# Performance work log

Hardware: AMD Instinct MI355X
Metric: run time of the kernel (lower is better)

The kernel has to match this reference:

```python
import jax, jax.numpy as jnp
import numpy as np

EMBED = 128; HEADS = 4; NUM_CLASSES = 20; NUM_LAYERS = 2
SCENE = (128, 128, 16)
NQ = SCENE[0] * SCENE[1] * SCENE[2]
NI = 300
IMG = (96, 320); ORI = (384, 1280)
VOXEL_SIZE = 0.2
SCORE_THR, MASK_THR, IOU_THR = 0.25, 0.5, 0.8


def _image_grid():
    # generate_grid(image_shape, ori_image_shape), then flip(dims=[0]) -> (x, y) pixel coords in ori resolution
    ys = jnp.arange(IMG[0], dtype=jnp.float32) * (ORI[0] / IMG[0])
    xs = jnp.arange(IMG[1], dtype=jnp.float32) * (ORI[1] / IMG[1])
    gy, gx = jnp.meshgrid(ys, xs, indexing='ij')
    return jnp.stack([gx, gy], 0)  # (2, h, w)


def _scene_pos():
    g = jnp.stack(jnp.meshgrid(*[jnp.arange(s, dtype=jnp.float32) for s in SCENE], indexing='ij'), 0)
    g = (g + 0.5) * VOXEL_SIZE  # project_scale = 1
    return g.reshape(3, -1).T  # (NQ, 3)


def _layernorm(x, g, b):
    mu = x.mean(-1, keepdims=True)
    var = ((x - mu) ** 2).mean(-1, keepdims=True)
    return (x - mu) * jax.lax.rsqrt(var + 1e-5) * g + b


def _mha(q, k, v, w, b):
    # w: (4, D, D) = Wq, Wk, Wv, Wo; b: (4, D)
    B, Nq, D = q.shape; hd = D // HEADS
    def proj(x, i):
        return (x @ w[i].T + b[i]).reshape(B, -1, HEADS, hd).transpose(0, 2, 1, 3)
    qh, kh, vh = proj(q, 0), proj(k, 1), proj(v, 2)
    attn = jax.nn.softmax(jnp.einsum('bhqd,bhkd->bhqk', qh, kh) / jnp.sqrt(jnp.float32(hd)), axis=-1)
    o = jnp.einsum('bhqk,bhkd->bhqd', attn, vh).transpose(0, 2, 1, 3).reshape(B, Nq, D)
    return o @ w[3].T + b[3]


def _tlayer(q, k, v, aw, ab, lg, lb, w1, b1, w2, b2):
    x = _layernorm(q + _mha(q, k, v, aw, ab), lg[0], lb[0])
    h = jax.nn.relu(x @ w1.T + b1) @ w2.T + b2
    return _layernorm(x + h, lg[1], lb[1])


def setup_inputs():
    key = jax.random.key(0)
    ks = jax.random.split(key, 20)
    h, w = IMG
    queries = jax.random.normal(ks[0], (1, NI, EMBED), jnp.float32)
    # 8 instances get a strong class logit so exactly they pass score_thr
    pred_logits = 0.1 * jax.random.normal(ks[1], (1, NI, NUM_CLASSES + 1), jnp.float32)
    ii = jnp.arange(8)
    pred_logits = pred_logits.at[0, ii, ii % (NUM_CLASSES + 1)].add(6.0)
    # each kept instance owns a disjoint 40-px-wide strip -> passes IoU>=0.8
    pred_masks = -6.0 + 0.1 * jax.random.normal(ks[2], (1, NI, h, w), jnp.float32)
    strip = jnp.arange(w) // 40  # 0..7
    boost = 12.0 * (jnp.arange(NI)[:, None] == strip[None, :]).astype(jnp.float32)
    pred_masks = pred_masks + boost[None, :, None, :]
    x3d = 0.1 * jax.random.normal(ks[3], (1, EMBED) + SCENE, jnp.float32)
    depth = 1.0 + 49.0 * jax.random.uniform(ks[4], (1, h, w), jnp.float32)
    K = jnp.array([[[500.0, 0.0, 160.0], [0.0, 500.0, 48.0], [0.0, 0.0, 1.0]]], jnp.float32)
    E = jnp.array([[[1.0, 0.0, 0.0, 0.5], [0.0, 1.0, 0.0, 1.0], [0.0, 0.0, 1.0, 1.5], [0.0, 0.0, 0.0, 1.0]]], jnp.float32)
    voxel_origin = jnp.array([[[0.0, -12.8, -2.0]]], jnp.float32)
    fov_mask = jax.random.bernoulli(ks[5], 0.25, (1, NQ))
    L = NUM_LAYERS
    scene_embed_w = 0.02 * jax.random.normal(ks[6], (NQ, EMBED), jnp.float32)
    inst_pos_w = 0.02 * jax.random.normal(ks[7], (NI, EMBED), jnp.float32)
    pos_w = 0.02 * jax.random.normal(ks[8], (EMBED, 3), jnp.float32)
    conv_w = 0.05 * jax.random.normal(ks[9], (NUM_CLASSES, EMBED), jnp.float32)
    conv_b = jnp.zeros((NUM_CLASSES,), jnp.float32)
    attn_w = 0.05 * jax.random.normal(ks[10], (L, 2, 4, EMBED, EMBED), jnp.float32)
    attn_b = jnp.zeros((L, 2, 4, EMBED), jnp.float32)
    ln_g = jnp.ones((L, 2, 2, EMBED), jnp.float32)
    ln_b = jnp.zeros((L, 2, 2, EMBED), jnp.float32)
    ffn_w1 = 0.05 * jax.random.normal(ks[11], (L, 2, 4 * EMBED, EMBED), jnp.float32)
    ffn_b1 = jnp.zeros((L, 2, 4 * EMBED), jnp.float32)
    ffn_w2 = 0.05 * jax.random.normal(ks[12], (L, 2, EMBED, 4 * EMBED), jnp.float32)
    ffn_b2 = jnp.zeros((L, 2, EMBED), jnp.float32)
    return dict(queries=queries, pred_logits=pred_logits, pred_masks=pred_masks, x3d=x3d, depth=depth,
                K=K, E=E, voxel_origin=voxel_origin, fov_mask=fov_mask,
                scene_embed_w=scene_embed_w, inst_pos_w=inst_pos_w, pos_w=pos_w, conv_w=conv_w, conv_b=conv_b,
                attn_w=attn_w, attn_b=attn_b, ln_g=ln_g, ln_b=ln_b,
                ffn_w1=ffn_w1, ffn_b1=ffn_b1, ffn_w2=ffn_w2, ffn_b2=ffn_b2)


def reference(queries, pred_logits, pred_masks, x3d, depth, K, E, voxel_origin, fov_mask,
              scene_embed_w, inst_pos_w, pos_w, conv_w, conv_b,
              attn_w, attn_b, ln_g, ln_b, ffn_w1, ffn_b1, ffn_w2, ffn_b2):
    h, w = IMG
    # ---- panoptic_postprocess (bs == 1) ----
    sig = jax.nn.sigmoid(pred_logits[0])
    prob_cls = jax.nn.softmax(sig / 0.06, axis=-1)
    scores = prob_cls.max(-1); labels = prob_cls.argmax(-1)
    keep = (labels != prob_cls.shape[-1]) & (scores > SCORE_THR)
    kidx = jnp.nonzero(keep)[0]
    pm = jax.nn.sigmoid(pred_masks[0])[kidx]          # (k, h, w)
    sk = scores[kidx]
    mids = (sk[:, None, None] * pm).argmax(0)          # per-pixel winning instance
    masks = mids[None] == jnp.arange(pm.shape[0])[:, None, None]
    marea = masks.reshape(pm.shape[0], -1).sum(1)
    pmb = pm >= MASK_THR
    parea = pmb.reshape(pm.shape[0], -1).sum(1)
    masks = masks & pmb
    keep_ = (masks.reshape(pm.shape[0], -1).sum(1) > 0) & (marea / parea >= IOU_THR)
    sel = jnp.nonzero(keep_)[0]
    inst_masks = masks[sel]                             # (k2, h, w)
    k2idx = kidx[sel]                                   # final kept slots in [0, NI)
    # ---- gather_mask_pos (depth already at (h, w) -> interpolate is identity) ----
    ig = _image_grid()
    ig3 = jnp.concatenate([ig[None] * depth[:, None], depth[:, None]], axis=1)  # (1,3,h,w) = (x*d, y*d, d)
    cam = jnp.linalg.inv(K) @ ig3.reshape(1, 3, -1)
    homo = jnp.concatenate([cam, jnp.ones((1, 1, h * w), cam.dtype)], axis=1)
    world = (jnp.linalg.inv(E) @ homo)[0, :3].T        # (hw, 3)
    xyz = inst_masks.reshape(inst_masks.shape[0], -1).astype(world.dtype) @ world  # masked sum per instance
    mask_pos = xyz @ pos_w.T                            # Linear(3, embed, bias=False)
    inst_q = queries[0][k2idx][None]                    # (1, k2, D)
    inst_p = (inst_pos_w[k2idx] + mask_pos)[None]
    # ---- scene tokens ----
    scene_embed_full = scene_embed_w[None] + x3d.reshape(1, EMBED, NQ).transpose(0, 2, 1)
    qsrc = scene_embed_full
    fidx = jnp.nonzero(fov_mask[0])[0]
    se = scene_embed_full[:, fidx]
    sp = ((_scene_pos()[None] + voxel_origin)[:, fidx]) @ pos_w.T
    for i in range(NUM_LAYERS):
        inst_q = _tlayer(inst_q + inst_p, se + sp, se, attn_w[i, 0], attn_b[i, 0], ln_g[i, 0], ln_b[i, 0],
                         ffn_w1[i, 0], ffn_b1[i, 0], ffn_w2[i, 0], ffn_b2[i, 0])
        se = _tlayer(se + sp, inst_q + inst_p, inst_q, attn_w[i, 1], attn_b[i, 1], ln_g[i, 1], ln_b[i, 1],
                     ffn_w1[i, 1], ffn_b1[i, 1], ffn_w2[i, 1], ffn_b2[i, 1])
    # ---- index_fov_back_to_voxels + cls_head (project_scale==1 -> Identity + 1x1 Conv3d) ----
    full = qsrc.at[:, fidx].set(se)
    x3d_ = full.transpose(0, 2, 1).reshape(1, EMBED, *SCENE)
    out = jnp.einsum('bcxyz,oc->boxyz', x3d_, conv_w) + conv_b.reshape(1, -1, 1, 1, 1)
    return out
```

## Files before the change

### kernel.cpp

```cpp
#include <hip/hip_runtime.h>
#include <math.h>

#define EMBED 128
#define NCLS 21
#define NI_ 300
#define IMH 96
#define IMW 320
#define NPIX (IMH*IMW)
#define NQ 262144
#define NF_MAX 73728
#define INST_MAX 16
#define IH_MAX 64
#define RS32 0.17677669529663687f

#define S_NF 0
#define S_NK 1
#define S_NINST 2
#define S_NIH 3
#define S_INVK 8
#define S_INVE 24
#define S_KIDX 64
#define S_SKK 400
#define S_MAREA 768
#define S_PAREA 1088
#define S_AREA2 1408
#define S_XYZ 1728
#define S_SELJ 2656
#define S_K2 2688
#define S_FCNT 3072
#define S_FOFF 3328
#define S_INSTQ 4096
#define S_INSTP 6144
#define S_QIN 8192
#define S_QH 10240
#define S_XI 12288
#define S_KHB 16384
#define S_VHB 18432
#define S_QKT 20480
#define S_SB 28672
#define S_SUMV 28928
#define S_WSUM 29056

#define OFF_FIDX ((size_t)1<<20)
#define OFF_INV  ((size_t)2<<20)
#define OFF_W1T  ((size_t)3<<20)
#define OFF_W2T  (((size_t)3<<20) + 512*128*4)
#define OFF_SE   ((size_t)4<<20)
#define SE_BYTES ((size_t)NF_MAX*128*4)
#define OFF_A1   (OFF_SE + SE_BYTES)
#define OFF_A2   (OFF_A1 + SE_BYTES)
#define OFF_SC   (OFF_A2 + SE_BYTES)

__global__ __launch_bounds__(256) void k_init(const float* Km, const float* Em, float* ws){
  int* iw = (int*)ws;
  for (int i = threadIdx.x; i < 4096; i += 256) iw[i] = 0;
  __syncthreads();
  if (threadIdx.x == 0){
    float* fw = ws;
    const float* K = Km;
    float A = K[4]*K[8]-K[5]*K[7];
    float B = K[5]*K[6]-K[3]*K[8];
    float C = K[3]*K[7]-K[4]*K[6];
    float det = K[0]*A + K[1]*B + K[2]*C;
    float id = 1.0f/det;
    fw[S_INVK+0] = A*id;
    fw[S_INVK+1] = (K[2]*K[7]-K[1]*K[8])*id;
    fw[S_INVK+2] = (K[1]*K[5]-K[2]*K[4])*id;
    fw[S_INVK+3] = B*id;
    fw[S_INVK+4] = (K[0]*K[8]-K[2]*K[6])*id;
    fw[S_INVK+5] = (K[2]*K[3]-K[0]*K[5])*id;
    fw[S_INVK+6] = C*id;
    fw[S_INVK+7] = (K[1]*K[6]-K[0]*K[7])*id;
    fw[S_INVK+8] = (K[0]*K[4]-K[1]*K[3])*id;
    float M[4][8];
    for (int r=0;r<4;r++){ for(int c=0;c<4;c++){ M[r][c]=Em[r*4+c]; M[r][4+c]=(r==c)?1.f:0.f; } }
    for (int col=0; col<4; col++){
      int piv=col; float best=fabsf(M[col][col]);
      for (int r=col+1;r<4;r++){ float v=fabsf(M[r][col]); if(v>best){best=v;piv=r;} }
      if (piv!=col){ for(int c=0;c<8;c++){ float tmp=M[col][c]; M[col][c]=M[piv][c]; M[piv][c]=tmp; } }
      float inv=1.0f/M[col][col];
      for (int c=0;c<8;c++) M[col][c]*=inv;
      for (int r=0;r<4;r++){ if(r==col) continue; float f=M[r][col]; for(int c=0;c<8;c++) M[r][c]-=f*M[col][c]; }
    }
    for (int r=0;r<4;r++) for(int c=0;c<4;c++) fw[S_INVE+r*4+c]=M[r][4+c];
  }
}

__global__ __launch_bounds__(320) void k_score(const float* logits, float* ws){
  int* iw=(int*)ws; float* fw=ws;
  __shared__ float ssc[NI_];
  __shared__ int skp[NI_];
  int t=threadIdx.x;
  if (t < NI_){
    float v[NCLS]; float mx=-1e30f;
    for (int c=0;c<NCLS;c++){
      float l=logits[t*NCLS+c];
      float sg=1.0f/(1.0f+expf(-l));
      float x=sg/0.06f;
      v[c]=x; mx=fmaxf(mx,x);
    }
    float s=0.f;
    for (int c=0;c<NCLS;c++) s += expf(v[c]-mx);
    float score=1.0f/s;
    ssc[t]=score; skp[t]=(score>0.25f)?1:0;
  }
  __syncthreads();
  if (t==0){
    int nk=0;
    for (int i=0;i<NI_;i++){ if(skp[i]){ iw[S_KIDX+nk]=i; fw[S_SKK+nk]=ssc[i]; nk++; } }
    iw[S_NK]=nk;
  }
}

__global__ __launch_bounds__(256) void k_winner(const float* pmask, const float* depth, float* ws){
  int* iw=(int*)ws; float* fw=ws;
  int nk=iw[S_NK];
  if (nk>NI_) nk=NI_;
  __shared__ int s_pa[NI_], s_ma[NI_], s_a2[NI_];
  __shared__ float s_x[NI_], s_y[NI_], s_z[NI_];
  __shared__ int s_gi[NI_];
  __shared__ float s_sc[NI_];
  int t=threadIdx.x;
  int lane=t&63;
  for (int j=t;j<nk;j+=256){
    s_pa[j]=0; s_ma[j]=0; s_a2[j]=0;
    s_x[j]=0.f; s_y[j]=0.f; s_z[j]=0.f;
    s_gi[j]=iw[S_KIDX+j]; s_sc[j]=fw[S_SKK+j];
  }
  __syncthreads();
// ... 60 lines not shown
    fw[S_INSTP+idx]=instposw[gi*128+e]+mp;
  }
}

__global__ __launch_bounds__(256) void k_fov_count(const int* fov, float* ws){
  int* iw=(int*)ws;
  __shared__ int red[256];
  int t=threadIdx.x;
  int base=blockIdx.x*1024;
  int s=0;
  for (int k=0;k<4;k++) s += (fov[base+k*256+t]!=0)?1:0;
  red[t]=s; __syncthreads();
  for (int st=128;st>0;st>>=1){ if(t<st) red[t]+=red[t+st]; __syncthreads(); }
  if (t==0) iw[S_FCNT+blockIdx.x]=red[0];
}

__global__ void k_fov_scan(float* ws){
  int* iw=(int*)ws;
  if (threadIdx.x==0){
    int acc=0;
    for (int b=0;b<256;b++){ iw[S_FOFF+b]=acc; acc+=iw[S_FCNT+b]; }
    iw[S_NF]=(acc<NF_MAX)?acc:NF_MAX;
  }
}

__global__ __launch_bounds__(256) void k_fov_scatter(const int* fov, float* ws){
  int* iw=(int*)ws;
  int* fidx=(int*)((char*)ws+OFF_FIDX);
  int* invr=(int*)((char*)ws+OFF_INV);
  __shared__ int wsums[4];
  __shared__ int woff[4];
  __shared__ int cur;
  __shared__ int tot;
  int t=threadIdx.x; int w=t>>6; int lane=t&63;
  if (t==0) cur=iw[S_FOFF+blockIdx.x];
  __syncthreads();
  int base=blockIdx.x*1024;
  for (int k=0;k<4;k++){
    int i=base+k*256+t;
    int f=(fov[i]!=0)?1:0;
    unsigned long long m=__ballot(f);
    int rk=__popcll(m & ((lane==0)?0ull:((~0ull)>>(64-lane))));
    if (lane==0) wsums[w]=__popcll(m);
    __syncthreads();
    if (t==0){ int a=0; for(int q2=0;q2<4;q2++){ woff[q2]=a; a+=wsums[q2]; } tot=a; }
    __syncthreads();
    if (f){
      int r=cur+woff[w]+rk;
      if (r<NF_MAX){ fidx[r]=i; invr[i]=r; } else invr[i]=-1;
    } else invr[i]=-1;
    __syncthreads();
    if (t==0) cur+=tot;
    __syncthreads();
  }
}

__global__ __launch_bounds__(256) void k_se_build(const float* sew, const float* x3d, const int* fidx, float* SE, float* ws){
  int* iw=(int*)ws;
  int nf=iw[S_NF];
  int r0=blockIdx.x*64;
  if (r0>=nf) return;
  int nr=min(64,nf-r0);
  __shared__ float tile[64][129];
  __shared__ int fidxl[64];
  int t=threadIdx.x;
  if (t<64) fidxl[t]=(t<nr)? fidx[r0+t]:0;
  __syncthreads();
  for (int idx=t; idx<64*128; idx+=256){
    int v=idx>>7, e=idx&127;
    tile[v][e]=(v<nr)? sew[(size_t)fidxl[v]*128+e]:0.f;
  }
  __syncthreads();
  for (int idx=t; idx<128*64; idx+=256){
    int c=idx>>6, v=idx&63;
    if (v<nr) tile[v][c]+=x3d[(size_t)c*NQ+fidxl[v]];
  }
  __syncthreads();
  for (int idx=t; idx<64*128; idx+=256){
    int v=idx>>7, e=idx&127;
    if (v<nr) SE[(r0+v)*128+e]=tile[v][e];
  }
}

__global__ __launch_bounds__(256) void kA_prep(const float* Wq, const float* bq, const float* Wk, const float* bk, float* ws){
  int* iw=(int*)ws; float* fw=ws;
  int n=iw[S_NINST]; int nih=iw[S_NIH];
  int t=threadIdx.x;
  for (int idx=t; idx<n*128; idx+=256) fw[S_QIN+idx]=fw[S_INSTQ+idx]+fw[S_INSTP+idx];
  __syncthreads();
  for (int idx=t; idx<n*128; idx+=256){
    int i=idx>>7, e=idx&127;
    float a=bq[e];
    for (int k=0;k<128;k++) a+=fw[S_QIN+i*128+k]*Wq[e*128+k];
    fw[S_QH+idx]=a;
  }
  __syncthreads();
  for (int idx=t; idx<nih*128; idx+=256){
    int ih=idx>>7, e=idx&127;
    int i=ih>>2, h=ih&3;
    float a=0.f;
    for (int d=0;d<32;d++) a+=fw[S_QH+i*128+h*32+d]*Wk[(h*32+d)*128+e];
    fw[S_QKT+idx]=a*RS32;
  }
  for (int ih=t; ih<nih; ih+=256){
    int i=ih>>2, h=ih&3;
    float a=0.f;
    for (int d=0;d<32;d++) a+=fw[S_QH+i*128+h*32+d]*bk[h*32+d];
    fw[S_SB+ih]=a*RS32;
  }
}

__global__ __launch_bounds__(256) void kS1(const float* SE, float* SC, const float* posw, const float* org, const int* fidx, float* ws){
  int* iw=(int*)ws; float* fw=ws;
  int nf=iw[S_NF]; int nih=iw[S_NIH];
  int r0=blockIdx.x*64;
  if (r0>=nf || nih==0) return;
  int nr=min(64,nf-r0);
  __shared__ float xt[64][132];
  __shared__ float qk[64][132];
  __shared__ float sbl[64];
  __shared__ float pwl[384];
  __shared__ float px[64],py[64],pz[64];
  __shared__ int fidxl[64];
  int t=threadIdx.x;
  for (int i=t;i<384;i+=256) pwl[i]=posw[i];
  if (t<64) fidxl[t]=(t<nr)? fidx[r0+t]:0;
  for (int idx=t; idx<64*32; idx+=256){
    int ih=idx>>5, e4=(idx&31)*4;
    float4 v = (ih<nih)? *reinterpret_cast<const float4*>(&fw[S_QKT+ih*128+e4])
                       : make_float4(0.f,0.f,0.f,0.f);
    *reinterpret_cast<float4*>(&qk[ih][e4]) = v;
  }
  if (t<64) sbl[t]=(t<nih)? fw[S_SB+t]:0.f;
  __syncthreads();
  if (t<64){
    int q=fidxl[t];
    int vx=q>>11, vy=(q>>4)&127, vz=q&15;
    px[t]=(vx+0.5f)*0.2f+org[0];
    py[t]=(vy+0.5f)*0.2f+org[1];
    pz[t]=(vz+0.5f)*0.2f+org[2];
  }
  __syncthreads();
  for (int idx=t; idx<64*32; idx+=256){
    int v=idx>>5, e4=(idx&31)*4;
    float4 s=make_float4(0.f,0.f,0.f,0.f);
    if (v<nr){
      s=*reinterpret_cast<const float4*>(SE+(size_t)(r0+v)*128+e4);
      float X=px[v], Y=py[v], Z=pz[v];
      s.x+=X*pwl[(e4+0)*3]+Y*pwl[(e4+0)*3+1]+Z*pwl[(e4+0)*3+2];
      s.y+=X*pwl[(e4+1)*3]+Y*pwl[(e4+1)*3+1]+Z*pwl[(e4+1)*3+2];
      s.z+=X*pwl[(e4+2)*3]+Y*pwl[(e4+2)*3+1]+Z*pwl[(e4+2)*3+2];
      s.w+=X*pwl[(e4+3)*3]+Y*pwl[(e4+3)*3+1]+Z*pwl[(e4+3)*3+2];
    }
    *reinterpret_cast<float4*>(&xt[v][e4])=s;
  }
  __syncthreads();
  int tx=t&15, ty=t>>4;
  int ih0=ty*4;
  float acc[4][4];
  #pragma unroll
  for (int i=0;i<4;i++)
    #pragma unroll
    for (int j=0;j<4;j++) acc[i][j]=0.f;
  for (int k=0;k<128;k+=4){
    float4 q0=*reinterpret_cast<const float4*>(&qk[ih0+0][k]);
    float4 q1=*reinterpret_cast<const float4*>(&qk[ih0+1][k]);
    float4 q2=*reinterpret_cast<const float4*>(&qk[ih0+2][k]);
    float4 q3=*reinterpret_cast<const float4*>(&qk[ih0+3][k]);
    #pragma unroll
    for (int j=0;j<4;j++){
      float4 x=*reinterpret_cast<const float4*>(&xt[tx+16*j][k]);
      acc[0][j]+=q0.x*x.x+q0.y*x.y+q0.z*x.z+q0.w*x.w;
      acc[1][j]+=q1.x*x.x+q1.y*x.y+q1.z*x.z+q1.w*x.w;
      acc[2][j]+=q2.x*x.x+q2.y*x.y+q2.z*x.z+q2.w*x.w;
      acc[3][j]+=q3.x*x.x+q3.y*x.y+q3.z*x.z+q3.w*x.w;
    }
  }
  #pragma unroll
  for (int i=0;i<4;i++){
    int ih=ih0+i;
    if (ih>=nih) break;
    float sb=sbl[ih];
    #pragma unroll
    for (int j=0;j<4;j++){
      int tok=tx+16*j;
      if (tok<nr) SC[(size_t)ih*NF_MAX+r0+tok]=acc[i][j]+sb;
    }
  }
}

__global__ __launch_bounds__(256) void kS2S3(float* SC, float* ws){
  int* iw=(int*)ws; float* fw=ws;
  int nih=iw[S_NIH]; int ih=blockIdx.x;
  if (ih>=nih) return;
  int nf=iw[S_NF];
  float* row=SC+(size_t)ih*NF_MAX;
  __shared__ float red[256];
  int t=threadIdx.x;
  float m=-1e30f;
  for (int j=t;j<nf;j+=256) m=fmaxf(m,row[j]);
  red[t]=m; __syncthreads();
  for (int s=128;s>0;s>>=1){ if(t<s) red[t]=fmaxf(red[t],red[t+s]); __syncthreads(); }
  m=red[0]; __syncthreads();
  float sum=0.f;
  for (int j=t;j<nf;j+=256){ float p=expf(row[j]-m); row[j]=p; sum+=p; }
  red[t]=sum; __syncthreads();
  for (int s=128;s>0;s>>=1){ if(t<s) red[t]+=red[t+s]; __syncthreads(); }
  if (t==0) fw[S_SUMV+ih]=red[0];
  if (t<128) fw[S_WSUM+ih*128+t]=0.f;
}

__global__ __launch_bounds__(256) void kS4(const float* __restrict__ SC, const float* __restrict__ SE, float* __restrict__ ws){
  int* iw=(int*)ws; float* fw=ws;
  int nf=iw[S_NF]; int nih=iw[S_NIH];
  if (nih==0) return;
  int t=threadIdx.x;
  int chunk=(nf+255)/256;
  int j0=blockIdx.x*chunk;
  int j1=min(nf,j0+chunk);
  if (j0>=j1) return;
  int tx=t&15, ty=t>>4;
  int ecol=tx*8, ih0=ty*4;
  const float* sc0=SC+(size_t)(ih0+0)*NF_MAX;
  const float* sc1=SC+(size_t)(ih0+1)*NF_MAX;
  const float* sc2=SC+(size_t)(ih0+2)*NF_MAX;
  const float* sc3=SC+(size_t)(ih0+3)*NF_MAX;
  bool g0=ih0+0<nih, g1=ih0+1<nih, g2=ih0+2<nih, g3=ih0+3<nih;
  float acc[4][8];
  #pragma unroll
  for (int i=0;i<4;i++)
    #pragma unroll
    for (int j=0;j<8;j++) acc[i][j]=0.f;
  #pragma unroll 4
  for (int j=j0;j<j1;j++){
    float4 sa=*reinterpret_cast<const float4*>(SE+(size_t)j*128+ecol);
    float4 sb=*reinterpret_cast<const float4*>(SE+(size_t)j*128+ecol+4);
    float s0=g0? sc0[j]:0.f;
    float s1=g1? sc1[j]:0.f;
    float s2=g2? sc2[j]:0.f;
    float s3=g3? sc3[j]:0.f;
    acc[0][0]+=s0*sa.x; acc[0][1]+=s0*sa.y; acc[0][2]+=s0*sa.z; acc[0][3]+=s0*sa.w;
    acc[0][4]+=s0*sb.x; acc[0][5]+=s0*sb.y; acc[0][6]+=s0*sb.z; acc[0][7]+=s0*sb.w;
    acc[1][0]+=s1*sa.x; acc[1][1]+=s1*sa.y; acc[1][2]+=s1*sa.z; acc[1][3]+=s1*sa.w;
    acc[1][4]+=s1*sb.x; acc[1][5]+=s1*sb.y; acc[1][6]+=s1*sb.z; acc[1][7]+=s1*sb.w;
    acc[2][0]+=s2*sa.x; acc[2][1]+=s2*sa.y; acc[2][2]+=s2*sa.z; acc[2][3]+=s2*sa.w;
    acc[2][4]+=s2*sb.x; acc[2][5]+=s2*sb.y; acc[2][6]+=s2*sb.z; acc[2][7]+=s2*sb.w;
    acc[3][0]+=s3*sa.x; acc[3][1]+=s3*sa.y; acc[3][2]+=s3*sa.z; acc[3][3]+=s3*sa.w;
    acc[3][4]+=s3*sb.x; acc[3][5]+=s3*sb.y; acc[3][6]+=s3*sb.z; acc[3][7]+=s3*sb.w;
  }
  #pragma unroll
  for (int i=0;i<4;i++){
    int ih=ih0+i;
    if (ih>=nih) break;
    #pragma unroll
    for (int jj=0;jj<8;jj++)
      atomicAdd(&fw[S_WSUM+ih*128+ecol+jj], acc[i][jj]);
  }
}

__global__ __launch_bounds__(256) void kA_post(const float* Wv, const float* bv, const float* Wo, const float* bo,
    const float* g, const float* bb, float* ws){
  int* iw=(int*)ws; float* fw=ws;
  int n=iw[S_NINST]; int nih=iw[S_NIH];
  __shared__ float wn[IH_MAX*128];
  __shared__ float ol[INST_MAX*128];
  __shared__ float tl[INST_MAX*128];
  int t=threadIdx.x;
  for (int idx=t; idx<nih*128; idx+=256){
    int ih=idx>>7;
    wn[idx]=fw[S_WSUM+idx]/fw[S_SUMV+ih];
  }
  __syncthreads();
  for (int idx=t; idx<n*128; idx+=256){
    int i=idx>>7, f=idx&127; int h=f>>5;
    float a=bv[f];
    const float* wrow=Wv+f*128;
    const float* wv=wn+(i*4+h)*128;
    for (int e2=0;e2<128;e2++) a+=wrow[e2]*wv[e2];
    ol[idx]=a;
  }
  __syncthreads();
  for (int idx=t; idx<n*128; idx+=256){
    int i=idx>>7, e2=idx&127;
    float a=bo[e2];
    const float* orow=ol+i*128;
    const float* wrow=Wo+e2*128;
    for (int f2=0;f2<128;f2++) a+=orow[f2]*wrow[f2];
    tl[idx]=a+fw[S_QIN+idx];
  }
  __syncthreads();
  int w=t>>6, lane=t&63;
  for (int i=w;i<n;i+=4){
    float v0=tl[i*128+lane], v1=tl[i*128+64+lane];
    float s=v0+v1;
    for (int o=32;o>0;o>>=1) s+=__shfl_xor(s,o);
    float mu=s*(1.f/128.f);
    float d0=v0-mu, d1=v1-mu;
    float vv=d0*d0+d1*d1;
    for (int o=32;o>0;o>>=1) vv+=__shfl_xor(vv,o);
    float rsv=rsqrtf(vv*(1.f/128.f)+1e-5f);
    fw[S_XI+i*128+lane]=d0*rsv*g[lane]+bb[lane];
    fw[S_XI+i*128+64+lane]=d1*rsv*g[64+lane]+bb[64+lane];
  }
}

__global__ __launch_bounds__(256) void kA_ffn(const float* W1, const float* b1, const float* W2, const float* b2,
    const float* g, const float* bb, float* ws){
  int* iw=(int*)ws; float* fw=ws;
  int n=iw[S_NINST];
  int i=blockIdx.x;
  if (i>=n) return;
  __shared__ float xl[128];
  __shared__ float hid[512];
  __shared__ float yv[128];
  int t=threadIdx.x;
  if (t<128) xl[t]=fw[S_XI+i*128+t];
  __syncthreads();
  for (int d=t; d<512; d+=256){
    float a=b1[d];
    const float* wr=W1+d*128;
    for (int k=0;k<128;k++) a+=wr[k]*xl[k];
    hid[d]=fmaxf(a,0.f);
  }
  __syncthreads();
  if (t<128){
    float a=b2[t];
    const float* wr=W2+(size_t)t*512;
    for (int d=0;d<512;d++) a+=wr[d]*hid[d];
    yv[t]=a+xl[t];
  }
  __syncthreads();
  if (t<64){
    float v0=yv[t], v1=yv[t+64];
    float s=v0+v1;
    for (int o=32;o>0;o>>=1) s+=__shfl_xor(s,o);
    float mu=s*(1.f/128.f);
    float d0=v0-mu, d1=v1-mu;
    float vv=d0*d0+d1*d1;
    for (int o=32;o>0;o>>=1) vv+=__shfl_xor(vv,o);
    float rsv=rsqrtf(vv*(1.f/128.f)+1e-5f);
    fw[S_INSTQ+i*128+t]=d0*rsv*g[t]+bb[t];
    fw[S_INSTQ+i*128+64+t]=d1*rsv*g[64+t]+bb[64+t];
  }
}

__global__ __launch_bounds__(256) void kA_kv(const float* Wk2, const float* bk2, const float* Wv2, const float* bv2, float* ws){
  int* iw=(int*)ws; float* fw=ws;
  int n=iw[S_NINST];
  int t=threadIdx.x;
  for (int idx=t; idx<n*128; idx+=256){
    int i=idx>>7, e=idx&127;
    float ak=bk2[e], av=bv2[e];
    const float* wk=Wk2+e*128;
    const float* wv=Wv2+e*128;
    for (int k=0;k<128;k++){
      float qv=fw[S_INSTQ+i*128+k];
      float qp=qv+fw[S_INSTP+i*128+k];
      ak+=qp*wk[k];
      av+=qv*wv[k];
    }
    fw[S_KHB+idx]=ak; fw[S_VHB+idx]=av;
  }
}

__global__ __launch_bounds__(256) void kQ(float* __restrict__ A1,
    const float* __restrict__ Wq, const float* __restrict__ bq,
    const float* __restrict__ SE, const int* __restrict__ fidx,
    const float* __restrict__ posw, const float* __restrict__ org, float* __restrict__ ws){
  int* iw=(int*)ws;
  int nf=iw[S_NF];
  int r0=blockIdx.x*64;
  if (r0>=nf) return;
  __shared__ float Xs[64][132];
  __shared__ float pwl[384];
  __shared__ float px[64],py[64],pz[64];
  int t=threadIdx.x;
  for (int i=t;i<384;i+=256) pwl[i]=posw[i];
  if (t<64){
    int r=r0+t;
    int q=(r<nf)? fidx[r]:0;
    int vx=q>>11, vy=(q>>4)&127, vz=q&15;
    px[t]=(vx+0.5f)*0.2f+org[0];
    py[t]=(vy+0.5f)*0.2f+org[1];
    pz[t]=(vz+0.5f)*0.2f+org[2];
  }
  __syncthreads();
  for (int idx=t; idx<64*32; idx+=256){
    int rl=idx>>5, e4=(idx&31)*4;
    float4 v=*reinterpret_cast<const float4*>(SE+(size_t)(r0+rl)*128+e4);
    float X=px[rl], Y=py[rl], Z=pz[rl];
    v.x+=X*pwl[(e4+0)*3]+Y*pwl[(e4+0)*3+1]+Z*pwl[(e4+0)*3+2];
    v.y+=X*pwl[(e4+1)*3]+Y*pwl[(e4+1)*3+1]+Z*pwl[(e4+1)*3+2];
    v.z+=X*pwl[(e4+2)*3]+Y*pwl[(e4+2)*3+1]+Z*pwl[(e4+2)*3+2];
    v.w+=X*pwl[(e4+3)*3]+Y*pwl[(e4+3)*3+1]+Z*pwl[(e4+3)*3+2];
    *reinterpret_cast<float4*>(&Xs[rl][e4])=v;
  }
  __syncthreads();
  int tx=t&15, ty=t>>4, ty4=ty*4, ecol=tx*8;
  float acc[4][8];
  #pragma unroll
  for (int i=0;i<4;i++)
    #pragma unroll
    for (int j=0;j<8;j++) acc[i][j]=0.f;
  for (int k=0;k<128;k+=4){
    float4 xv0=*reinterpret_cast<const float4*>(&Xs[ty4+0][k]);
    float4 xv1=*reinterpret_cast<const float4*>(&Xs[ty4+1][k]);
    float4 xv2=*reinterpret_cast<const float4*>(&Xs[ty4+2][k]);
    float4 xv3=*reinterpret_cast<const float4*>(&Xs[ty4+3][k]);
    #pragma unroll
    for (int jj=0;jj<8;jj++){
      float4 w=*reinterpret_cast<const float4*>(Wq+(size_t)(ecol+jj)*128+k);
      acc[0][jj]+=xv0.x*w.x+xv0.y*w.y+xv0.z*w.z+xv0.w*w.w;
      acc[1][jj]+=xv1.x*w.x+xv1.y*w.y+xv1.z*w.z+xv1.w*w.w;
      acc[2][jj]+=xv2.x*w.x+xv2.y*w.y+xv2.z*w.z+xv2.w*w.w;
      acc[3][jj]+=xv3.x*w.x+xv3.y*w.y+xv3.z*w.z+xv3.w*w.w;
    }
  }
  float4 bqa=*reinterpret_cast<const float4*>(bq+ecol);
  float4 bqb=*reinterpret_cast<const float4*>(bq+ecol+4);
  #pragma unroll
  for (int i=0;i<4;i++){
    int r=r0+ty4+i;
    if (r>=nf) continue;
    float4 o1, o2;
    o1.x=acc[i][0]+bqa.x; o1.y=acc[i][1]+bqa.y; o1.z=acc[i][2]+bqa.z; o1.w=acc[i][3]+bqa.w;
    o2.x=acc[i][4]+bqb.x; o2.y=acc[i][5]+bqb.y; o2.z=acc[i][6]+bqb.z; o2.w=acc[i][7]+bqb.w;
    *reinterpret_cast<float4*>(A1+(size_t)r*128+ecol)=o1;
    *reinterpret_cast<float4*>(A1+(size_t)r*128+ecol+4)=o2;
  }
}

__global__ __launch_bounds__(256) void kAttnOLN(const float* __restrict__ A1, float* __restrict__ A2,
    const float* __restrict__ Wo, const float* __restrict__ bo,
    const float* __restrict__ g, const float* __restrict__ bb,
    const float* __restrict__ SE, const int* __restrict__ fidx,
    const float* __restrict__ posw, const float* __restrict__ org, float* __restrict__ ws){
  int* iw=(int*)ws; float* fw=ws;
  int nf=iw[S_NF]; int n=iw[S_NINST];
  int r0=blockIdx.x*64;
  if (r0>=nf) return;
  __shared__ float ot[64][132];
  __shared__ float kh[INST_MAX*128];
  __shared__ float vh[INST_MAX*128];
  __shared__ float pwl[384];
// ... 249 lines not shown
    for (int o=32;o>0;o>>=1) vv+=__shfl_xor(vv,o);
    float rsv=rsqrtf(vv*(1.f/128.f)+1e-5f);
    if (r<nf){
      SEo[r*128+lane]=d0*rsv*g[lane]+bb[lane];
      SEo[r*128+64+lane]=d1*rsv*g[64+lane]+bb[64+lane];
    }
  }
}

__global__ __launch_bounds__(256) void k_out(const float* SE, const float* sew, const float* x3d,
    const float* convw, const float* convb, const int* invr, float* out, float* ws){
  (void)ws;
  __shared__ float rows[64][132];
  __shared__ float cw[20*128];
  __shared__ float cb[20];
  __shared__ int rkl[64];
  int t=threadIdx.x;
  int q0=blockIdx.x*64;
  for (int idx=t; idx<20*128; idx+=256) cw[idx]=convw[idx];
  if (t<20) cb[t]=convb[t];
  if (t<64) rkl[t]=invr[q0+t];
  __syncthreads();
  for (int idx=t; idx<64*32; idx+=256){
    int v=idx>>5, e4=(idx&31)*4;
    int rk=rkl[v];
    float4 val = (rk>=0)? *reinterpret_cast<const float4*>(SE+(size_t)rk*128+e4)
                        : *reinterpret_cast<const float4*>(sew+(size_t)(q0+v)*128+e4);
    *reinterpret_cast<float4*>(&rows[v][e4])=val;
  }
  __syncthreads();
  for (int idx=t; idx<128*64; idx+=256){
    int c=idx>>6, v=idx&63;
    if (rkl[v]<0) rows[v][c]+=x3d[(size_t)c*NQ+q0+v];
  }
  __syncthreads();
  int v=t&63, slot=t>>6;
  float acc[5]={0.f,0.f,0.f,0.f,0.f};
  for (int c=0;c<128;c+=4){
    float4 rv=*reinterpret_cast<const float4*>(&rows[v][c]);
    #pragma unroll
    for (int oo=0;oo<5;oo++){
      float4 cv=*reinterpret_cast<const float4*>(&cw[(slot*5+oo)*128+c]);
      acc[oo]+=rv.x*cv.x+rv.y*cv.y+rv.z*cv.z+rv.w*cv.w;
    }
  }
  #pragma unroll
  for (int oo=0;oo<5;oo++){
    int o=slot*5+oo;
    out[(size_t)o*NQ+q0+v]=acc[oo]+cb[o];
  }
}

extern "C" void kernel_launch(void* const* d_in, const int* in_sizes, int n_in,
                              void* d_out, int out_size, void* d_ws, size_t ws_size,
                              hipStream_t stream){
  (void)in_sizes; (void)n_in; (void)out_size; (void)ws_size;
  const float* queries  = (const float*)d_in[0];
  const float* plogits  = (const float*)d_in[1];
  const float* pmasks   = (const float*)d_in[2];
  const float* x3d      = (const float*)d_in[3];
  const float* depth    = (const float*)d_in[4];
  const float* Kmat     = (const float*)d_in[5];
  const float* Emat     = (const float*)d_in[6];
  const float* vorigin  = (const float*)d_in[7];
  const int*   fov      = (const int*)d_in[8];
  const float* sew      = (const float*)d_in[9];
  const float* instposw = (const float*)d_in[10];
  const float* posw     = (const float*)d_in[11];
  const float* convw    = (const float*)d_in[12];
  const float* convb    = (const float*)d_in[13];
  const float* AW       = (const float*)d_in[14];
  const float* AB       = (const float*)d_in[15];
  const float* LG       = (const float*)d_in[16];
  const float* LB       = (const float*)d_in[17];
  const float* F1W      = (const float*)d_in[18];
  const float* F1B      = (const float*)d_in[19];
  const float* F2W      = (const float*)d_in[20];
  const float* F2B      = (const float*)d_in[21];
  float* out = (float*)d_out;
  char* wsb = (char*)d_ws;
  float* fws = (float*)d_ws;
  int* fidx = (int*)(wsb + OFF_FIDX);
  int* invr = (int*)(wsb + OFF_INV);
  float* W1T = (float*)(wsb + OFF_W1T);
  float* W2T = (float*)(wsb + OFF_W2T);
  float* SE = (float*)(wsb + OFF_SE);
  float* A1 = (float*)(wsb + OFF_A1);
  float* A2 = (float*)(wsb + OFF_A2);
  float* SC = (float*)(wsb + OFF_SC);

  auto aw  = [&](int i,int br,int m){ return AW + (size_t)(((i*2+br)*4+m))*128*128; };
  auto ab  = [&](int i,int br,int m){ return AB + (size_t)(((i*2+br)*4+m))*128; };
  auto lng = [&](int i,int br,int wch){ return LG + (size_t)(((i*2+br)*2+wch))*128; };
  auto lnb = [&](int i,int br,int wch){ return LB + (size_t)(((i*2+br)*2+wch))*128; };
  auto f1w = [&](int i,int br){ return F1W + (size_t)(i*2+br)*512*128; };
  auto f1b = [&](int i,int br){ return F1B + (size_t)(i*2+br)*512; };
  auto f2w = [&](int i,int br){ return F2W + (size_t)(i*2+br)*128*512; };
  auto f2b = [&](int i,int br){ return F2B + (size_t)(i*2+br)*128; };

  const int NB64 = NF_MAX/64;

  k_init<<<1,256,0,stream>>>(Kmat,Emat,fws);
  k_score<<<1,320,0,stream>>>(plogits,fws);
  k_winner<<<NPIX/256,256,0,stream>>>(pmasks,depth,fws);
  k_sel<<<1,256,0,stream>>>(queries,instposw,posw,fws);
  k_fov_count<<<256,256,0,stream>>>(fov,fws);
  k_fov_scan<<<1,64,0,stream>>>(fws);
  k_fov_scatter<<<256,256,0,stream>>>(fov,fws);
  k_se_build<<<NB64,256,0,stream>>>(sew,x3d,fidx,SE,fws);

  for (int i=0;i<2;i++){
    kA_prep<<<1,256,0,stream>>>(aw(i,0,0),ab(i,0,0),aw(i,0,1),ab(i,0,1),fws);
    kS1<<<NB64,256,0,stream>>>(SE,SC,posw,vorigin,fidx,fws);
    kS2S3<<<IH_MAX,256,0,stream>>>(SC,fws);
    kS4<<<256,256,0,stream>>>(SC,SE,fws);
    kA_post<<<1,256,0,stream>>>(aw(i,0,2),ab(i,0,2),aw(i,0,3),ab(i,0,3),lng(i,0,0),lnb(i,0,0),fws);
    kA_ffn<<<INST_MAX,256,0,stream>>>(f1w(i,0),f1b(i,0),f2w(i,0),f2b(i,0),lng(i,0,1),lnb(i,0,1),fws);
    kA_kv<<<1,256,0,stream>>>(aw(i,1,1),ab(i,1,1),aw(i,1,2),ab(i,1,2),fws);
    kQ<<<NB64,256,0,stream>>>(A1,aw(i,1,0),ab(i,1,0),SE,fidx,posw,vorigin,fws);
    kAttnOLN<<<NB64,256,0,stream>>>(A1,A2,aw(i,1,3),ab(i,1,3),lng(i,1,0),lnb(i,1,0),SE,fidx,posw,vorigin,fws);
    k_transpose<<<dim3(4,16),dim3(32,8),0,stream>>>(f1w(i,1),W1T,512,128);
    k_transpose<<<dim3(16,4),dim3(32,8),0,stream>>>(f2w(i,1),W2T,128,512);
    kFFN<<<NB64,256,0,stream>>>(A2,SE,W1T,W2T,f1b(i,1),f2b(i,1),lng(i,1,1),lnb(i,1,1),fws);
  }
  k_out<<<NQ/64,256,0,stream>>>(SE,sew,x3d,convw,convb,invr,out,fws);
}
```

Before: 2.567 ms.

## Fuse instance-branch tail kernels and parallelize instance query prep across blocks

Merges the instance attention output projection, layernorm, FFN, second layernorm and the K/V projection for the scene branch into one per-instance kernel. kA_prep now runs one block per instance-head instead of a single block, and its matvecs use float4 loads. Both layers' FFN weight transposes move ahead of the layer loop into separate buffers. The goal is to cut serial single-block kernels and launch count on the small instance path. kA_prep recomputes the query projection redundantly in every block, and QIN/QH are no longer written to the workspace, so any other reader of those would break.

```diff
diff --git a/kernel.cpp b/kernel.cpp
--- a/kernel.cpp
+++ b/kernel.cpp
@@ -44,7 +44,6 @@
 #define OFF_FIDX ((size_t)1<<20)
 #define OFF_INV  ((size_t)2<<20)
 #define OFF_W1T  ((size_t)3<<20)
-#define OFF_W2T  (((size_t)3<<20) + 512*128*4)
 #define OFF_SE   ((size_t)4<<20)
 #define SE_BYTES ((size_t)NF_MAX*128*4)
 #define OFF_A1   (OFF_SE + SE_BYTES)
@@ -271,31 +270,42 @@
   }
 }
 
-__global__ __launch_bounds__(256) void kA_prep(const float* Wq, const float* bq, const float* Wk, const float* bk, float* ws){
+__global__ __launch_bounds__(256) void kA_prep(const float* __restrict__ Wq, const float* __restrict__ bq,
+    const float* __restrict__ Wk, const float* __restrict__ bk, float* __restrict__ ws){
   int* iw=(int*)ws; float* fw=ws;
   int n=iw[S_NINST]; int nih=iw[S_NIH];
-  int t=threadIdx.x;
-  for (int idx=t; idx<n*128; idx+=256) fw[S_QIN+idx]=fw[S_INSTQ+idx]+fw[S_INSTP+idx];
+  int b=blockIdx.x;
+  if (b>=nih) return;
+  int t=threadIdx.x;
+  __shared__ __attribute__((aligned(16))) float qin[INST_MAX*128];
+  __shared__ __attribute__((aligned(16))) float qh[INST_MAX*128];
+  for (int idx=t; idx<n*128; idx+=256)
+    qin[idx]=fw[S_INSTQ+idx]+fw[S_INSTP+idx];
   __syncthreads();
   for (int idx=t; idx<n*128; idx+=256){
     int i=idx>>7, e=idx&127;
     float a=bq[e];
-    for (int k=0;k<128;k++) a+=fw[S_QIN+i*128+k]*Wq[e*128+k];
-    fw[S_QH+idx]=a;
-  }
-  __syncthreads();
-  for (int idx=t; idx<nih*128; idx+=256){
-    int ih=idx>>7, e=idx&127;
-    int i=ih>>2, h=ih&3;
+    const float4* wr=reinterpret_cast<const float4*>(Wq+(size_t)e*128);
+    const float4* xr=reinterpret_cast<const float4*>(qin+i*128);
+    #pragma unroll 8
+    for (int k4=0;k4<32;k4++){
+      float4 w=wr[k4]; float4 x=xr[k4];
+      a+=x.x*w.x+x.y*w.y+x.z*w.z+x.w*w.w;
+    }
+    qh[idx]=a;
+  }
+  __syncthreads();
+  int i=b>>2, h=b&3;
+  const float* qs=qh+i*128+h*32;
+  if (t<128){
     float a=0.f;
-    for (int d=0;d<32;d++) a+=fw[S_QH+i*128+h*32+d]*Wk[(h*32+d)*128+e];
-    fw[S_QKT+idx]=a*RS32;
-  }
-  for (int ih=t; ih<nih; ih+=256){
-    int i=ih>>2, h=ih&3;
+    #pragma unroll 8
+    for (int d=0;d<32;d++) a+=qs[d]*Wk[(size_t)(h*32+d)*128+t];
+    fw[S_QKT+b*128+t]=a*RS32;
+  } else if (t==128){
     float a=0.f;
-    for (int d=0;d<32;d++) a+=fw[S_QH+i*128+h*32+d]*bk[h*32+d];
-    fw[S_SB+ih]=a*RS32;
+    for (int d=0;d<32;d++) a+=qs[d]*bk[h*32+d];
+    fw[S_SB+b]=a*RS32;
   }
 }
 
@@ -447,40 +457,60 @@
   }
 }
 
-__global__ __launch_bounds__(256) void kA_post(const float* Wv, const float* bv, const float* Wo, const float* bo,
-    const float* g, const float* bb, float* ws){
+__global__ __launch_bounds__(256) void kA_tail(
+    const float* __restrict__ Wv, const float* __restrict__ bv,
+    const float* __restrict__ Wo, const float* __restrict__ bo,
+    const float* __restrict__ g0, const float* __restrict__ bb0,
+    const float* __restrict__ W1, const float* __restrict__ b1,
+    const float* __restrict__ W2, const float* __restrict__ b2,
+    const float* __restrict__ g1, const float* __restrict__ bb1,
+    const float* __restrict__ Wk2, const float* __restrict__ bk2,
+    const float* __restrict__ Wv2, const float* __restrict__ bv2,
+    float* __restrict__ ws){
   int* iw=(int*)ws; float* fw=ws;
-  int n=iw[S_NINST]; int nih=iw[S_NIH];
-  __shared__ float wn[IH_MAX*128];
-  __shared__ float ol[INST_MAX*128];
-  __shared__ float tl[INST_MAX*128];
-  int t=threadIdx.x;
-  for (int idx=t; idx<nih*128; idx+=256){
-    int ih=idx>>7;
-    wn[idx]=fw[S_WSUM+idx]/fw[S_SUMV+ih];
-  }
-  __syncthreads();
-  for (int idx=t; idx<n*128; idx+=256){
-    int i=idx>>7, f=idx&127; int h=f>>5;
-    float a=bv[f];
-    const float* wrow=Wv+f*128;
-    const float* wv=wn+(i*4+h)*128;
-    for (int e2=0;e2<128;e2++) a+=wrow[e2]*wv[e2];
-    ol[idx]=a;
-  }
-  __syncthreads();
-  for (int idx=t; idx<n*128; idx+=256){
-    int i=idx>>7, e2=idx&127;
-    float a=bo[e2];
-    const float* orow=ol+i*128;
-    const float* wrow=Wo+e2*128;
-    for (int f2=0;f2<128;f2++) a+=orow[f2]*wrow[f2];
-    tl[idx]=a+fw[S_QIN+idx];
-  }
-  __syncthreads();
-  int w=t>>6, lane=t&63;
-  for (int i=w;i<n;i+=4){
-    float v0=tl[i*128+lane], v1=tl[i*128+64+lane];
+  int n=iw[S_NINST];
+  int i=blockIdx.x;
+  if (i>=n) return;
+  int t=threadIdx.x;
+  __shared__ __attribute__((aligned(16))) float wn4[4*128];
+  __shared__ __attribute__((aligned(16))) float ol[128];
+  __shared__ __attribute__((aligned(16))) float xi[128];
+  __shared__ __attribute__((aligned(16))) float hid[512];
+  __shared__ __attribute__((aligned(16))) float qrow[128];
+  __shared__ __attribute__((aligned(16))) float prow[128];
+  for (int idx=t; idx<512; idx+=256){
+    int ih=i*4+(idx>>7);
+    wn4[idx]=fw[S_WSUM+ih*128+(idx&127)]/fw[S_SUMV+ih];
+  }
+  if (t<128) prow[t]=fw[S_INSTP+i*128+t];
+  __syncthreads();
+  if (t<128){
+    int h=t>>5;
+    float a=bv[t];
+    const float4* wr=reinterpret_cast<const float4*>(Wv+(size_t)t*128);
+    const float4* xr=reinterpret_cast<const float4*>(wn4+h*128);
+    #pragma unroll 8
+    for (int k4=0;k4<32;k4++){
+      float4 w=wr[k4]; float4 x=xr[k4];
+      a+=x.x*w.x+x.y*w.y+x.z*w.z+x.w*w.w;
+    }
+    ol[t]=a;
+  }
+  __syncthreads();
+  if (t<128){
+    float a=bo[t];
+    const float4* wr=reinterpret_cast<const float4*>(Wo+(size_t)t*128);
+    const float4* xr=reinterpret_cast<const float4*>(ol);
+    #pragma unroll 8
+    for (int k4=0;k4<32;k4++){
+      float4 w=wr[k4]; float4 x=xr[k4];
+      a+=x.x*w.x+x.y*w.y+x.z*w.z+x.w*w.w;
+    }
+    xi[t]=a+fw[S_INSTQ+i*128+t]+prow[t];
+  }
+  __syncthreads();
+  if (t<64){
+    float v0=xi[t], v1=xi[t+64];
     float s=v0+v1;
     for (int o=32;o>0;o>>=1) s+=__shfl_xor(s,o);
     float mu=s*(1.f/128.f);
@@ -488,39 +518,36 @@
     float vv=d0*d0+d1*d1;
     for (int o=32;o>0;o>>=1) vv+=__shfl_xor(vv,o);
     float rsv=rsqrtf(vv*(1.f/128.f)+1e-5f);
-    fw[S_XI+i*128+lane]=d0*rsv*g[lane]+bb[lane];
-    fw[S_XI+i*128+64+lane]=d1*rsv*g[64+lane]+bb[64+lane];
-  }
-}
-
-__global__ __launch_bounds__(256) void kA_ffn(const float* W1, const float* b1, const float* W2, const float* b2,
-    const float* g, const float* bb, float* ws){
-  int* iw=(int*)ws; float* fw=ws;
-  int n=iw[S_NINST];
-  int i=blockIdx.x;
-  if (i>=n) return;
-  __shared__ float xl[128];
-  __shared__ float hid[512];
-  __shared__ float yv[128];
-  int t=threadIdx.x;
-  if (t<128) xl[t]=fw[S_XI+i*128+t];
+    xi[t]=d0*rsv*g0[t]+bb0[t];
+    xi[t+64]=d1*rsv*g0[t+64]+bb0[t+64];
+  }
   __syncthreads();
   for (int d=t; d<512; d+=256){
     float a=b1[d];
-    const float* wr=W1+d*128;
-    for (int k=0;k<128;k++) a+=wr[k]*xl[k];
+    const float4* wr=reinterpret_cast<const float4*>(W1+(size_t)d*128);
+    const float4* xr=reinterpret_cast<const float4*>(xi);
+    #pragma unroll 8
+    for (int k4=0;k4<32;k4++){
+      float4 w=wr[k4]; float4 x=xr[k4];
+      a+=x.x*w.x+x.y*w.y+x.z*w.z+x.w*w.w;
+    }
     hid[d]=fmaxf(a,0.f);
   }
   __syncthreads();
   if (t<128){
     float a=b2[t];
-    const float* wr=W2+(size_t)t*512;
-    for (int d=0;d<512;d++) a+=wr[d]*hid[d];
-    yv[t]=a+xl[t];
+    const float4* wr=reinterpret_cast<const float4*>(W2+(size_t)t*512);
+    const float4* xr=reinterpret_cast<const float4*>(hid);
+    #pragma unroll 8
+    for (int k4=0;k4<128;k4++){
+      float4 w=wr[k4]; float4 x=xr[k4];
+      a+=x.x*w.x+x.y*w.y+x.z*w.z+x.w*w.w;
+    }
+    qrow[t]=a+xi[t];
   }
   __syncthreads();
   if (t<64){
-    float v0=yv[t], v1=yv[t+64];
+    float v0=qrow[t], v1=qrow[t+64];
     float s=v0+v1;
     for (int o=32;o>0;o>>=1) s+=__shfl_xor(s,o);
     float mu=s*(1.f/128.f);
@@ -528,27 +555,35 @@
     float vv=d0*d0+d1*d1;
     for (int o=32;o>0;o>>=1) vv+=__shfl_xor(vv,o);
     float rsv=rsqrtf(vv*(1.f/128.f)+1e-5f);
-    fw[S_INSTQ+i*128+t]=d0*rsv*g[t]+bb[t];
-    fw[S_INSTQ+i*128+64+t]=d1*rsv*g[64+t]+bb[64+t];
-  }
-}
-
-__global__ __launch_bounds__(256) void kA_kv(const float* Wk2, const float* bk2, const float* Wv2, const float* bv2, float* ws){
-  int* iw=(int*)ws; float* fw=ws;
-  int n=iw[S_NINST];
-  int t=threadIdx.x;
-  for (int idx=t; idx<n*128; idx+=256){
-    int i=idx>>7, e=idx&127;
-    float ak=bk2[e], av=bv2[e];
-    const float* wk=Wk2+e*128;
-    const float* wv=Wv2+e*128;
-    for (int k=0;k<128;k++){
-      float qv=fw[S_INSTQ+i*128+k];
-      float qp=qv+fw[S_INSTP+i*128+k];
-      ak+=qp*wk[k];
-      av+=qv*wv[k];
-    }
-    fw[S_KHB+idx]=ak; fw[S_VHB+idx]=av;
+    qrow[t]=d0*rsv*g1[t]+bb1[t];
+    qrow[t+64]=d1*rsv*g1[t+64]+bb1[t+64];
+  }
+  __syncthreads();
+  if (t<128) fw[S_INSTQ+i*128+t]=qrow[t];
+  {
+    int e=t&127, which=t>>7;
+    if (which==0){
+      float a=bk2[e];
+      const float4* wr=reinterpret_cast<const float4*>(Wk2+(size_t)e*128);
+      #pragma unroll 8
+      for (int k4=0;k4<32;k4++){
+        float4 w=wr[k4];
+        float4 q4=*reinterpret_cast<const float4*>(qrow+k4*4);
+        float4 p4=*reinterpret_cast<const float4*>(prow+k4*4);
+        a+=(q4.x+p4.x)*w.x+(q4.y+p4.y)*w.y+(q4.z+p4.z)*w.z+(q4.w+p4.w)*w.w;
+      }
+      fw[S_KHB+i*128+e]=a;
+    } else {
+      float a=bv2[e];
+      const float4* wr=reinterpret_cast<const float4*>(Wv2+(size_t)e*128);
+      #pragma unroll 8
+      for (int k4=0;k4<32;k4++){
+        float4 w=wr[k4];
+        float4 q4=*reinterpret_cast<const float4*>(qrow+k4*4);
+        a+=q4.x*w.x+q4.y*w.y+q4.z*w.z+q4.w*w.w;
+      }
+      fw[S_VHB+i*128+e]=a;
+    }
   }
 }
 
@@ -964,12 +999,12 @@
   float* fws = (float*)d_ws;
   int* fidx = (int*)(wsb + OFF_FIDX);
   int* invr = (int*)(wsb + OFF_INV);
-  float* W1T = (float*)(wsb + OFF_W1T);
-  float* W2T = (float*)(wsb + OFF_W2T);
   float* SE = (float*)(wsb + OFF_SE);
   float* A1 = (float*)(wsb + OFF_A1);
   float* A2 = (float*)(wsb + OFF_A2);
   float* SC = (float*)(wsb + OFF_SC);
+  float* W1Ta[2] = { (float*)(wsb + OFF_W1T),              (float*)(wsb + OFF_W1T + 512*1024) };
+  float* W2Ta[2] = { (float*)(wsb + OFF_W1T + 256*1024),   (float*)(wsb + OFF_W1T + 768*1024) };
 
   auto aw  = [&](int i,int br,int m){ return AW + (size_t)(((i*2+br)*4+m))*128*128; };
   auto ab  = [&](int i,int br,int m){ return AB + (size_t)(((i*2+br)*4+m))*128; };
@@ -990,20 +1025,23 @@
   k_fov_scan<<<1,64,0,stream>>>(fws);
   k_fov_scatter<<<256,256,0,stream>>>(fov,fws);
   k_se_build<<<NB64,256,0,stream>>>(sew,x3d,fidx,SE,fws);
-
   for (int i=0;i<2;i++){
-    kA_prep<<<1,256,0,stream>>>(aw(i,0,0),ab(i,0,0),aw(i,0,1),ab(i,0,1),fws);
+    k_transpose<<<dim3(4,16),dim3(32,8),0,stream>>>(f1w(i,1),W1Ta[i],512,128);
+    k_transpose<<<dim3(16,4),dim3(32,8),0,stream>>>(f2w(i,1),W2Ta[i],128,512);
+  }
+
+  for (int i=0;i<2;i++){
+    kA_prep<<<IH_MAX,256,0,stream>>>(aw(i,0,0),ab(i,0,0),aw(i,0,1),ab(i,0,1),fws);
     kS1<<<NB64,256,0,stream>>>(SE,SC,posw,vorigin,fidx,fws);
     kS2S3<<<IH_MAX,256,0,stream>>>(SC,fws);
     kS4<<<256,256,0,stream>>>(SC,SE,fws);
-    kA_post<<<1,256,0,stream>>>(aw(i,0,2),ab(i,0,2),aw(i,0,3),ab(i,0,3),lng(i,0,0),lnb(i,0,0),fws);
-    kA_ffn<<<INST_MAX,256,0,stream>>>(f1w(i,0),f1b(i,0),f2w(i,0),f2b(i,0),lng(i,0,1),lnb(i,0,1),fws);
-    kA_kv<<<1,256,0,stream>>>(aw(i,1,1),ab(i,1,1),aw(i,1,2),ab(i,1,2),fws);
+    kA_tail<<<INST_MAX,256,0,stream>>>(
+      aw(i,0,2),ab(i,0,2), aw(i,0,3),ab(i,0,3), lng(i,0,0),lnb(i,0,0),
+      f1w(i,0),f1b(i,0), f2w(i,0),f2b(i,0), lng(i,0,1),lnb(i,0,1),
+      aw(i,1,1),ab(i,1,1), aw(i,1,2),ab(i,1,2), fws);
     kQ<<<NB64,256,0,stream>>>(A1,aw(i,1,0),ab(i,1,0),SE,fidx,posw,vorigin,fws);
     kAttnOLN<<<NB64,256,0,stream>>>(A1,A2,aw(i,1,3),ab(i,1,3),lng(i,1,0),lnb(i,1,0),SE,fidx,posw,vorigin,fws);
-    k_transpose<<<dim3(4,16),dim3(32,8),0,stream>>>(f1w(i,1),W1T,512,128);
-    k_transpose<<<dim3(16,4),dim3(32,8),0,stream>>>(f2w(i,1),W2T,128,512);
-    kFFN<<<NB64,256,0,stream>>>(A2,SE,W1T,W2T,f1b(i,1),f2b(i,1),lng(i,1,1),lnb(i,1,1),fws);
+    kFFN<<<NB64,256,0,stream>>>(A2,SE,W1Ta[i],W2Ta[i],f1b(i,1),f2b(i,1),lng(i,1,1),lnb(i,1,1),fws);
   }
   k_out<<<NQ/64,256,0,stream>>>(SE,sew,x3d,convw,convb,invr,out,fws);
 }
```

New measurement: 2.439 ms. -5.0%, faster.
